# Optimization experiments

Measured on AMD Instinct MI355X. Metric: run time of the kernel, lower is better.

The kernel has to match this reference:

```python
import jax, jax.numpy as jnp
import numpy as np

H = 16
QK_NOPE = 128
QK_ROPE = 64
QK_HEAD = 192
V_HEAD = 128
KV_LORA = 512
Q_LORA = 1536
HIDDEN = 2048
ROPE_THETA = 500000.0
EPS = 1e-6


def _rms_norm(x, w, eps=EPS):
    var = jnp.mean(x * x, axis=-1, keepdims=True)
    return w * (x * jax.lax.rsqrt(var + eps))


def _rotate_half(x):
    d = x.shape[-1] // 2
    return jnp.concatenate([-x[..., d:], x[..., :d]], axis=-1)


def _rope_cos_sin(T, dim, theta, dtype):
    inv_freq = 1.0 / (theta ** (jnp.arange(0, dim, 2, dtype=jnp.float32) / dim))
    t = jnp.arange(T, dtype=jnp.float32)
    freqs = jnp.outer(t, inv_freq)               # [T, dim//2]
    emb = jnp.concatenate([freqs, freqs], axis=-1)  # [T, dim]
    return jnp.cos(emb).astype(dtype), jnp.sin(emb).astype(dtype)


def _apply_rope_interleave(q, k, cos, sin):
    # deinterleave: [x0,x1,x2,...] -> [x0,x2,... , x1,x3,...]
    def deint(x):
        return jnp.concatenate([x[..., 0::2], x[..., 1::2]], axis=-1)
    q, k = deint(q), deint(k)
    cos = cos[None, None]  # [1,1,T,d]
    sin = sin[None, None]
    q_e = q * cos + _rotate_half(q) * sin
    k_e = k * cos + _rotate_half(k) * sin
    return q_e, k_e


def setup_inputs() -> dict:
    key = jax.random.key(0)
    ks = jax.random.split(key, 8)
    s = 0.02
    B, T = 2, 2048
    return {
        "x": jax.random.normal(ks[0], (B, T, HIDDEN), jnp.float32),
        "q_a_w": jax.random.normal(ks[1], (HIDDEN, Q_LORA), jnp.float32) * s,
        "q_a_ln_w": jnp.ones((Q_LORA,), jnp.float32),
        "q_b_w": jax.random.normal(ks[2], (Q_LORA, H * QK_HEAD), jnp.float32) * s,
        "kv_a_w": jax.random.normal(ks[3], (HIDDEN, KV_LORA + QK_ROPE), jnp.float32) * s,
        "kv_a_ln_w": jnp.ones((KV_LORA,), jnp.float32),
        "kv_b_w": jax.random.normal(ks[4], (KV_LORA, H * (QK_NOPE + V_HEAD)), jnp.float32) * s,
        "o_w": jax.random.normal(ks[5], (H * V_HEAD, HIDDEN), jnp.float32) * s,
    }


def reference(x, q_a_w, q_a_ln_w, q_b_w, kv_a_w, kv_a_ln_w, kv_b_w, o_w):
    B, T, _ = x.shape
    scale = QK_HEAD ** -0.5

    # Q path: hidden -> q_lora -> RMSNorm -> H*qk_head
    q = _rms_norm(x @ q_a_w, q_a_ln_w) @ q_b_w
    q = q.reshape(B, T, H, QK_HEAD).transpose(0, 2, 1, 3)  # [B,H,T,qk_head]
    q_nope, q_rope = q[..., :QK_NOPE], q[..., QK_NOPE:]

    # KV path: hidden -> kv_lora + rope_dim
    ckv = x @ kv_a_w
    kv_c, k_rope = ckv[..., :KV_LORA], ckv[..., KV_LORA:]
    kv = _rms_norm(kv_c, kv_a_ln_w) @ kv_b_w
    kv = kv.reshape(B, T, H, QK_NOPE + V_HEAD).transpose(0, 2, 1, 3)
    k_nope, v = kv[..., :QK_NOPE], kv[..., QK_NOPE:]

    k_rope = k_rope.reshape(B, 1, T, QK_ROPE)
    cos, sin = _rope_cos_sin(T, QK_ROPE, ROPE_THETA, x.dtype)
    q_rope, k_rope = _apply_rope_interleave(q_rope, k_rope, cos, sin)
    k_rope = jnp.broadcast_to(k_rope, (B, H, T, QK_ROPE))

    qf = jnp.concatenate([q_nope, q_rope], axis=-1)  # [B,H,T,192]
    kf = jnp.concatenate([k_nope, k_rope], axis=-1)

    # causal SDPA
    scores = jnp.einsum("bhqd,bhkd->bhqk", qf, kf) * scale
    causal = jnp.tril(jnp.ones((T, T), bool))
    scores = jnp.where(causal[None, None], scores, jnp.finfo(scores.dtype).min)
    attn = jax.nn.softmax(scores, axis=-1)
    out = jnp.einsum("bhqk,bhkd->bhqd", attn, v)  # [B,H,T,128]
    out = out.transpose(0, 2, 1, 3).reshape(B, T, H * V_HEAD)
    return out @ o_w
```

## Files before the change

### kernel.cpp

```cpp
#include <hip/hip_runtime.h>
#include <hip/hip_bf16.h>
#include <cstdint>


typedef __bf16 bf16;
typedef __bf16 bf16x8 __attribute__((ext_vector_type(8)));
typedef __bf16 bf16x4v __attribute__((ext_vector_type(4)));
typedef float f32x4 __attribute__((ext_vector_type(4)));

#define TSEQ 2048
#define MR 4096

typedef const uint32_t __attribute__((address_space(1))) * gas1_t;
typedef uint32_t __attribute__((address_space(3))) * las3_t;

static __device__ __forceinline__ void gload_lds16(const void* g, void* l) {
  __builtin_amdgcn_global_load_lds(
      reinterpret_cast<gas1_t>(reinterpret_cast<uintptr_t>(g)),
      reinterpret_cast<las3_t>(reinterpret_cast<uintptr_t>(l)), 16, 0, 0);
}

static __device__ __forceinline__ f32x4 mfma16(bf16x8 a, bf16x8 b, f32x4 c) {
  return __builtin_amdgcn_mfma_f32_16x16x32_bf16(a, b, c, 0, 0, 0);
}


__global__ __launch_bounds__(256) void k_cvt_bf16(const float* __restrict__ in,
                                                  bf16* __restrict__ out) {
  int i = blockIdx.x * 256 + threadIdx.x;
  float4 f = reinterpret_cast<const float4*>(in)[i];
  bf16x4v o = {(bf16)f.x, (bf16)f.y, (bf16)f.z, (bf16)f.w};
  reinterpret_cast<bf16x4v*>(out)[i] = o;
}

__global__ __launch_bounds__(256) void k_transpose(const float* __restrict__ W,
                                                   bf16* __restrict__ Wt,
                                                   int K, int N) {
  __shared__ float t[32][33];
  int bi = blockIdx.x, bj = blockIdx.y;
  int c = threadIdx.x & 31, r0 = threadIdx.x >> 5;
#pragma unroll
  for (int rr = 0; rr < 32; rr += 8)
    t[rr + r0][c] = W[(size_t)(bj * 32 + rr + r0) * N + bi * 32 + c];
  __syncthreads();
#pragma unroll
  for (int rr = 0; rr < 32; rr += 8)
    Wt[(size_t)(bi * 32 + rr + r0) * K + bj * 32 + c] = (bf16)t[c][rr + r0];
}

__global__ __launch_bounds__(64) void k_rope_table(float* __restrict__ rt) {
  int t = blockIdx.x * 2 + (threadIdx.x >> 5);
  int j = threadIdx.x & 31;
  float freq = exp2f(-(float)j * (1.0f / 32.0f) * log2f(500000.0f));
  float ang = (float)t * freq;
  rt[t * 64 + 2 * j] = cosf(ang);
  rt[t * 64 + 2 * j + 1] = sinf(ang);
}

template <int NCH>
__global__ __launch_bounds__(64) void k_rmsnorm(const bf16* __restrict__ in,
                                                const float* __restrict__ w,
                                                bf16* __restrict__ out,
                                                int in_stride) {
  int row = blockIdx.x, lane = threadIdx.x;
  const int D = NCH * 512;
  const bf16* ip = in + (size_t)row * in_stride;
  bf16x8 v[NCH];
  float ss = 0.f;
#pragma unroll
  for (int c = 0; c < NCH; ++c) {
    v[c] = *reinterpret_cast<const bf16x8*>(ip + c * 512 + lane * 8);
#pragma unroll
    for (int e = 0; e < 8; ++e) { float f = (float)v[c][e]; ss += f * f; }
  }
#pragma unroll
  for (int m = 1; m <= 32; m <<= 1) ss += __shfl_xor(ss, m);
  float rs = rsqrtf(ss / (float)D + 1e-6f);
  bf16* op = out + (size_t)row * D;
#pragma unroll
  for (int c = 0; c < NCH; ++c) {
    bf16x8 o;
#pragma unroll
    for (int e = 0; e < 8; ++e)
      o[e] = (bf16)((float)v[c][e] * rs * w[c * 512 + lane * 8 + e]);
    *reinterpret_cast<bf16x8*>(op + c * 512 + lane * 8) = o;
  }
}

__global__ __launch_bounds__(64) void k_kv_norm_rope(
    const bf16* __restrict__ in, const float* __restrict__ w,
    const float* __restrict__ rt, bf16* __restrict__ kvn,
    bf16* __restrict__ kr, int in_stride) {
  int row = blockIdx.x, lane = threadIdx.x;
  const bf16* ip = in + (size_t)row * in_stride;
  bf16x8 v = *reinterpret_cast<const bf16x8*>(ip + lane * 8);
  float ss = 0.f;
#pragma unroll
  for (int e = 0; e < 8; ++e) { float f = (float)v[e]; ss += f * f; }
#pragma unroll
  for (int m = 1; m <= 32; m <<= 1) ss += __shfl_xor(ss, m);
  float rs = rsqrtf(ss / 512.0f + 1e-6f);
  bf16x8 o;
#pragma unroll
  for (int e = 0; e < 8; ++e) o[e] = (bf16)((float)v[e] * rs * w[lane * 8 + e]);
  *reinterpret_cast<bf16x8*>(kvn + (size_t)row * 512 + lane * 8) = o;
  if (lane < 32) {
    int t = row & (TSEQ - 1);
    float x0 = (float)ip[512 + 2 * lane], x1 = (float)ip[512 + 2 * lane + 1];
    float c = rt[t * 64 + 2 * lane], s = rt[t * 64 + 2 * lane + 1];
    kr[(size_t)row * 64 + lane] = (bf16)(x0 * c - x1 * s);
    kr[(size_t)row * 64 + 32 + lane] = (bf16)(x1 * c + x0 * s);
  }
}

__global__ __launch_bounds__(256) void k_rope_q(const bf16* __restrict__ q,
                                                const float* __restrict__ rt,
                                                bf16* __restrict__ qr) {
  int idx = blockIdx.x * 256 + threadIdx.x;
  int j = idx & 31, h = (idx >> 5) & 15, row = idx >> 9;
  int t = row & (TSEQ - 1);
  const bf16* src = q + (size_t)row * 3072 + h * 192 + 128;
  float x0 = (float)src[2 * j], x1 = (float)src[2 * j + 1];
  float c = rt[t * 64 + 2 * j], s = rt[t * 64 + 2 * j + 1];
  bf16* dst = qr + ((size_t)row * 16 + h) * 64;
  dst[j] = (bf16)(x0 * c - x1 * s);
  dst[32 + j] = (bf16)(x1 * c + x0 * s);
}

template <bool OUT_F32>
__global__ __launch_bounds__(256) void k_gemm_bt(const bf16* __restrict__ A,
                                                 const bf16* __restrict__ Bt,
                                                 void* __restrict__ C, int M,
                                                 int N, int K) {
  __shared__ bf16 As[128 * 32];
  __shared__ bf16 Bs[128 * 32];
  const int tid = threadIdx.x, lane = tid & 63, w = tid >> 6;
  const int wm = w >> 1, wn = w & 1;
  const int lg = lane >> 4, lr = lane & 15;
  const int m0 = blockIdx.y * 128, n0 = blockIdx.x * 128;
  f32x4 acc[4][4] = {};
  for (int k0 = 0; k0 < K; k0 += 32) {
    __syncthreads();
#pragma unroll
    for (int i = 0; i < 2; ++i) {
      int chunk = i * 256 + w * 64 + lane;
      int row = chunk >> 2, cc = chunk & 3;
      gload_lds16(A + (size_t)(m0 + row) * K + k0 + cc * 8,
                  (char*)As + (size_t)(i * 256 + w * 64) * 16);
      int nr = n0 + row;
      nr = nr < N ? nr : N - 1;
      gload_lds16(Bt + (size_t)nr * K + k0 + cc * 8,
                  (char*)Bs + (size_t)(i * 256 + w * 64) * 16);
    }
    __syncthreads();
    bf16x8 af[4], bfr[4];
#pragma unroll
    for (int mi = 0; mi < 4; ++mi)
      af[mi] = *reinterpret_cast<const bf16x8*>(
          &As[(wm * 64 + mi * 16 + lr) * 32 + lg * 8]);
#pragma unroll
    for (int ni = 0; ni < 4; ++ni)
      bfr[ni] = *reinterpret_cast<const bf16x8*>(
          &Bs[(wn * 64 + ni * 16 + lr) * 32 + lg * 8]);
#pragma unroll
    for (int mi = 0; mi < 4; ++mi)
#pragma unroll
      for (int ni = 0; ni < 4; ++ni)
        acc[mi][ni] = mfma16(af[mi], bfr[ni], acc[mi][ni]);
  }
#pragma unroll
  for (int mi = 0; mi < 4; ++mi)
#pragma unroll
    for (int ni = 0; ni < 4; ++ni) {
      int col = n0 + wn * 64 + ni * 16 + lr;
      if (col < N) {
#pragma unroll
        for (int r = 0; r < 4; ++r) {
          int rowg = m0 + wm * 64 + mi * 16 + lg * 4 + r;
          if (OUT_F32)
            reinterpret_cast<float*>(C)[(size_t)rowg * N + col] = acc[mi][ni][r];
          else
            reinterpret_cast<bf16*>(C)[(size_t)rowg * N + col] =
                (bf16)acc[mi][ni][r];
        }
      }
    }
}

#define GPH(BUF, MH, KH, DO_READB, STAGE_STMT, WAIT_STMT)                     \
  {                                                                           \
    if (DO_READB) {                                                           \
      _Pragma("unroll") for (int ni = 0; ni < 4; ++ni) {                      \
        int row = wn * 64 + ni * 16 + lr;                                     \
        breg[KH][ni] = *reinterpret_cast<const bf16x8*>(                      \
            &Bs[BUF][row * 64 + ((((KH)*4 + lg) ^ (row & 7)) * 8)]);          \
      }                                                                       \
    }                                                                         \
    bf16x8 af[4];                                                             \
    _Pragma("unroll") for (int mi = 0; mi < 4; ++mi) {                        \
      int row = wm * 128 + (MH)*64 + mi * 16 + lr;                            \
      af[mi] = *reinterpret_cast<const bf16x8*>(                              \
          &As[BUF][row * 64 + ((((KH)*4 + lg) ^ (row & 7)) * 8)]);            \
    }                                                                         \
    STAGE_STMT;                                                               \
    __builtin_amdgcn_s_barrier();                                             \
    __builtin_amdgcn_s_setprio(1);                                            \
    _Pragma("unroll") for (int mi = 0; mi < 4; ++mi)                          \
        _Pragma("unroll") for (int ni = 0; ni < 4; ++ni)                      \
            acc[(MH)*4 + mi][ni] =                                            \
        mfma16(af[mi], breg[KH][ni], acc[(MH)*4 + mi][ni]);                   \
    __builtin_amdgcn_s_setprio(0);                                            \
    WAIT_STMT;                                                                \
    __builtin_amdgcn_s_barrier();                                             \
  }

template <bool OUT_F32>
__global__ __launch_bounds__(512, 2) void k_gemm8(const bf16* __restrict__ A,
                                                  const bf16* __restrict__ Bt,
                                                  void* __restrict__ C, int M,
                                                  int N, int K) {
  __shared__ bf16 As[2][256 * 64];
  __shared__ bf16 Bs[2][256 * 64];
  const int tid = threadIdx.x, lane = tid & 63, w = tid >> 6;
  const int lg = lane >> 4, lr = lane & 15;
  const int wm = w >> 2, wn = w & 3;
  const int m0 = blockIdx.y * 256, n0 = blockIdx.x * 256;
  const int T = K >> 7;

  f32x4 acc[8][4] = {};
  bf16x8 breg[2][4];

  auto stageA = [&](int tau, int h) {
    char* dst = (char*)&As[tau & 1][0] + h * 16384;
#pragma unroll
    for (int j = 0; j < 2; ++j) {
      int c = j * 512 + tid;
      int row = c >> 3, slot = c & 7;
      gload_lds16(A + (size_t)(m0 + h * 128 + row) * K + tau * 64 +
                      ((slot ^ (row & 7)) * 8),
                  dst + (size_t)(j * 512 + w * 64) * 16);
    }
  };
  auto stageB = [&](int tau, int h) {
    char* dst = (char*)&Bs[tau & 1][0] + h * 16384;
#pragma unroll
    for (int j = 0; j < 2; ++j) {
      int c = j * 512 + tid;
      int row = c >> 3, slot = c & 7;
      gload_lds16(Bt + (size_t)(n0 + h * 128 + row) * K + tau * 64 +
                      ((slot ^ (row & 7)) * 8),
                  dst + (size_t)(j * 512 + w * 64) * 16);
    }
  };

  stageB(0, 0); stageB(0, 1); stageA(0, 0); stageA(0, 1);
  stageB(1, 0); stageB(1, 1); stageA(1, 0);
  asm volatile("s_waitcnt vmcnt(6)" ::: "memory");
  __builtin_amdgcn_s_barrier();

  for (int t = 0; t < T - 1; ++t) {
    const int s2 = 2 * t + 2, s3 = 2 * t + 3, a1 = 2 * t + 1;
    GPH(0, 0, 0, true,  stageA(a1, 1), ((void)0));
    GPH(0, 0, 1, true,  stageB(s2, 0), ((void)0));
    GPH(0, 1, 0, false, stageB(s2, 1), ((void)0));
    GPH(0, 1, 1, false, stageA(s2, 0),
        asm volatile("s_waitcnt vmcnt(6)" ::: "memory"));
    GPH(1, 0, 0, true,  stageA(s2, 1), ((void)0));
    GPH(1, 0, 1, true,  stageB(s3, 0), ((void)0));
    GPH(1, 1, 0, false, stageB(s3, 1), ((void)0));
    GPH(1, 1, 1, false, stageA(s3, 0),
        asm volatile("s_waitcnt vmcnt(6)" ::: "memory"));
  }
  {
    const int a1 = 2 * T - 1;
    GPH(0, 0, 0, true,  stageA(a1, 1), ((void)0));
    GPH(0, 0, 1, true,  ((void)0),     ((void)0));
    GPH(0, 1, 0, false, ((void)0),     ((void)0));
    GPH(0, 1, 1, false, ((void)0),
        asm volatile("s_waitcnt vmcnt(0)" ::: "memory"));
    GPH(1, 0, 0, true,  ((void)0), ((void)0));
    GPH(1, 0, 1, true,  ((void)0), ((void)0));
    GPH(1, 1, 0, false, ((void)0), ((void)0));
    GPH(1, 1, 1, false, ((void)0), ((void)0));
  }

#pragma unroll
  for (int mi = 0; mi < 8; ++mi)
#pragma unroll
    for (int ni = 0; ni < 4; ++ni) {
      int col = n0 + wn * 64 + ni * 16 + lr;
#pragma unroll
      for (int r = 0; r < 4; ++r) {
        int rowg = m0 + wm * 128 + mi * 16 + lg * 4 + r;
        if (OUT_F32)
          reinterpret_cast<float*>(C)[(size_t)rowg * N + col] = acc[mi][ni][r];
        else
          reinterpret_cast<bf16*>(C)[(size_t)rowg * N + col] =
              (bf16)acc[mi][ni][r];
      }
    }
}

__global__ __launch_bounds__(512, 2) void k_attn(const bf16* __restrict__ q,
                                                 const bf16* __restrict__ qr,
                                                 const bf16* __restrict__ kv,
                                                 const bf16* __restrict__ kr,
                                                 bf16* __restrict__ o) {
  __shared__ bf16 Kn[2][64 * 128];
  __shared__ bf16 Kr[2][64 * 64];
  __shared__ bf16 Vs[2][64 * 128];
  __shared__ bf16 Ps[8 * 1024];
  const int tid = threadIdx.x, lane = tid & 63, w = tid >> 6;
  const int lg = lane >> 4, lr = lane & 15;
  const float qsc = 0.07216878364870323f * 1.44269504088896f;
  uint4 vreg[2];
  const int vrr = tid & 31, vvc = tid >> 5;

  for (int t = 0; t < 2; ++t) {
    const int id = t ? 511 - (int)blockIdx.x : (int)blockIdx.x;
    const int qt = 15 - (id >> 5);
    const int bh = id & 31;
    const int b = bh >> 4, h = bh & 15;
    const int q0 = qt * 128;
    const size_t rowbase = (size_t)b * TSEQ;
    const int nkt = 2 * qt + 2;
    const int qg = q0 + w * 16 + lr;

    auto issue_loads = [&](int kbase, int buf) {
#pragma unroll
      for (int kk = 0; kk < 2; ++kk)
        vreg[kk] = *reinterpret_cast<const uint4*>(
            kv + (rowbase + kbase + vrr * 2 + kk) * 4096 + h * 256 + 128 +
            vvc * 8);
#pragma unroll
      for (int i = 0; i < 2; ++i) {
        int c = i * 512 + tid;
        int row = c >> 4, j = c & 15;
        gload_lds16(
            kv + (rowbase + kbase + row) * 4096 + h * 256 +
                ((j ^ (row & 15)) * 8),
            (char*)&Kn[buf][0] + (size_t)(i * 512 + w * 64) * 16);
      }
      {
        int row = tid >> 3, j = tid & 7;
        gload_lds16(kr + (rowbase + kbase + row) * 64 + ((j ^ (row & 7)) * 8),
                    (char*)&Kr[buf][0] + (size_t)(w * 64) * 16);
      }
    };

    auto write_vs = [&](int buf) {
      const int kb0 = vrr * 2;
      const int cC = kb0 >> 5, g = (kb0 >> 3) & 3, j0 = kb0 & 7;
      const uint32_t* r0 = reinterpret_cast<const uint32_t*>(&vreg[0]);
      const uint32_t* r1 = reinterpret_cast<const uint32_t*>(&vreg[1]);
#pragma unroll
      for (int e = 0; e < 8; ++e) {
        uint32_t h0 = (r0[e >> 1] >> ((e & 1) * 16)) & 0xffffu;
        uint32_t h1 = (r1[e >> 1] >> ((e & 1) * 16)) & 0xffffu;
        int vd = vvc * 8 + e;
        int slot = (vd & 15) ^ g;
        *reinterpret_cast<uint32_t*>(
            &Vs[buf][((cC * 8 + (vd >> 4)) * 4 + g) * 128 + slot * 8 + j0]) =
            h0 | (h1 << 16);
      }
    };

    bf16x8 qf[6];
    {
      const bf16* qp = q + (rowbase + qg) * 3072 + h * 192;
#pragma unroll
      for (int dc = 0; dc < 4; ++dc) {
        bf16x8 v = *reinterpret_cast<const bf16x8*>(qp + dc * 32 + lg * 8);
#pragma unroll
        for (int e = 0; e < 8; ++e) v[e] = (bf16)((float)v[e] * qsc);
        qf[dc] = v;
      }
      const bf16* qrp = qr + ((rowbase + qg) * 16 + h) * 64;
#pragma unroll
      for (int dc = 0; dc < 2; ++dc) {
        bf16x8 v = *reinterpret_cast<const bf16x8*>(qrp + dc * 32 + lg * 8);
#pragma unroll
        for (int e = 0; e < 8; ++e) v[e] = (bf16)((float)v[e] * qsc);
        qf[4 + dc] = v;
      }
    }

    f32x4 oacc[8] = {};
    float m_run = -1e30f, l_run = 0.f;

    issue_loads(0, 0);
    write_vs(0);
    __syncthreads();

    for (int kt = 0; kt < nkt; ++kt) {
      const int kbase = kt * 64;
      const int buf = kt & 1;
      const bool more = (kt + 1 < nkt);
      if (more) issue_loads(kbase + 64, buf ^ 1);

      if (kbase <= q0 + w * 16 + 15) {
        f32x4 sacc[4];
#pragma unroll
        for (int kb = 0; kb < 4; ++kb) {
          const int row = kb * 16 + lr;
          bf16x8 kf[6];
#pragma unroll
          for (int dc = 0; dc < 4; ++dc)
            kf[dc] = *reinterpret_cast<const bf16x8*>(
                &Kn[buf][row * 128 + (((dc * 4 + lg) ^ (row & 15)) * 8)]);
#pragma unroll
          for (int dc = 0; dc < 2; ++dc)
            kf[4 + dc] = *reinterpret_cast<const bf16x8*>(
                &Kr[buf][row * 64 + (((dc * 4 + lg) ^ (row & 7)) * 8)]);
          __builtin_amdgcn_s_setprio(1);
          f32x4 sa = {0.f, 0.f, 0.f, 0.f};
#pragma unroll
          for (int dc = 0; dc < 6; ++dc) sa = mfma16(kf[dc], qf[dc], sa);
          sacc[kb] = sa;
          __builtin_amdgcn_s_setprio(0);
        }
        float sv[4][4];
        float pmax = -1e30f;
#pragma unroll
        for (int kb = 0; kb < 4; ++kb)
#pragma unroll
          for (int r = 0; r < 4; ++r) {
            int kgl = kbase + kb * 16 + lg * 4 + r;
            float val = (kgl <= qg) ? sacc[kb][r] : -1e30f;
            sv[kb][r] = val;
            pmax = fmaxf(pmax, val);
          }
        pmax = fmaxf(pmax, __shfl_xor(pmax, 16));
        pmax = fmaxf(pmax, __shfl_xor(pmax, 32));
        float mnew = fmaxf(m_run, pmax);
        float alpha = exp2f(m_run - mnew);
        float ls = 0.f;
#pragma unroll
        for (int kb = 0; kb < 4; ++kb) {
          bf16x4v pw;
#pragma unroll
          for (int r = 0; r < 4; ++r) {
            float p = exp2f(sv[kb][r] - mnew);
            ls += p;
            pw[r] = (bf16)p;
          }
          *reinterpret_cast<bf16x4v*>(
              &Ps[w * 1024 + lr * 64 +
                  (((kb * 2 + (lg >> 1)) ^ (lr & 7)) * 8) + (lg & 1) * 4]) = pw;
        }
        ls += __shfl_xor(ls, 16);
        ls += __shfl_xor(ls, 32);
        l_run = l_run * alpha + ls;
        m_run = mnew;
#pragma unroll
        for (int vb = 0; vb < 8; ++vb) {
          oacc[vb][0] *= alpha; oacc[vb][1] *= alpha;
          oacc[vb][2] *= alpha; oacc[vb][3] *= alpha;
        }
#pragma unroll
        for (int c = 0; c < 2; ++c) {
          bf16x8 pb = *reinterpret_cast<const bf16x8*>(
              &Ps[w * 1024 + lr * 64 + (((c * 4 + lg) ^ (lr & 7)) * 8)]);
          __builtin_amdgcn_s_setprio(1);
#pragma unroll
          for (int vb = 0; vb < 8; ++vb) {
            bf16x8 av = *reinterpret_cast<const bf16x8*>(
                &Vs[buf][((c * 8 + vb) * 4 + lg) * 128 + (lr ^ lg) * 8]);
            oacc[vb] = mfma16(av, pb, oacc[vb]);
          }
          __builtin_amdgcn_s_setprio(0);
        }
      }
      if (more) write_vs(buf ^ 1);
      __syncthreads();
    }

    bf16* Os = &Kn[0][0] + w * 2048;
    {
      float inv = 1.0f / l_run;
#pragma unroll
      for (int vb = 0; vb < 8; ++vb) {
        bf16x4v ov;
#pragma unroll
        for (int r = 0; r < 4; ++r) ov[r] = (bf16)(oacc[vb][r] * inv);
        int slot16 = vb * 2 + (lg >> 1);
        *reinterpret_cast<bf16x4v*>(
            &Os[lr * 128 + ((slot16 ^ (lr & 7)) * 8) + (lg & 1) * 4]) = ov;
      }
    }
    asm volatile("s_waitcnt lgkmcnt(0)");
    __builtin_amdgcn_sched_barrier(0);
#pragma unroll
    for (int i = 0; i < 4; ++i) {
      const int r = i * 4 + lg;
      bf16x8 ov = *reinterpret_cast<const bf16x8*>(
          &Os[r * 128 + ((lr ^ (r & 7)) * 8)]);
      *reinterpret_cast<bf16x8*>(
          o + (rowbase + q0 + w * 16 + r) * 2048 + h * 128 + lr * 8) = ov;
    }
    __syncthreads();
  }
}

extern "C" void kernel_launch(void* const* d_in, const int* in_sizes, int n_in,
                              void* d_out, int out_size, void* d_ws,
                              size_t ws_size, hipStream_t stream) {
  (void)in_sizes; (void)n_in; (void)out_size; (void)ws_size;
  const float* x       = (const float*)d_in[0];
  const float* q_a_w   = (const float*)d_in[1];
  const float* q_a_ln  = (const float*)d_in[2];
  const float* q_b_w   = (const float*)d_in[3];
  const float* kv_a_w  = (const float*)d_in[4];
  const float* kv_a_ln = (const float*)d_in[5];
  const float* kv_b_w  = (const float*)d_in[6];
  const float* o_w     = (const float*)d_in[7];

  char* ws = (char*)d_ws;
  size_t off = 0;
  auto alloc = [&](size_t bytes) {
    void* p = ws + off;
    off += (bytes + 255) & ~(size_t)255;
    return p;
  };
  bf16* x_bf   = (bf16*)alloc((size_t)MR * 2048 * 2);
  bf16* ab_wt  = (bf16*)alloc((size_t)2112 * 2048 * 2);
  bf16* qb_wt  = (bf16*)alloc((size_t)3072 * 1536 * 2);
  bf16* kvb_wt = (bf16*)alloc((size_t)4096 * 512 * 2);
  bf16* o_wt   = (bf16*)alloc((size_t)2048 * 2048 * 2);
  float* rt    = (float*)alloc((size_t)2048 * 64 * 4);
  bf16* qac    = (bf16*)alloc((size_t)MR * 2112 * 2);
  bf16* q_a_n  = (bf16*)alloc((size_t)MR * 1536 * 2);
  bf16* kv_c_n = (bf16*)alloc((size_t)MR * 512 * 2);
  bf16* kr     = (bf16*)alloc((size_t)MR * 64 * 2);
  bf16* qbuf   = (bf16*)alloc((size_t)MR * 3072 * 2);
  bf16* qr     = (bf16*)alloc((size_t)MR * 16 * 64 * 2);
  bf16* kvbuf  = (bf16*)alloc((size_t)MR * 4096 * 2);
  bf16* attn_o = (bf16*)alloc((size_t)MR * 2048 * 2);

  k_cvt_bf16<<<8192, 256, 0, stream>>>(x, x_bf);
  k_transpose<<<dim3(1536 / 32, 2048 / 32), 256, 0, stream>>>(q_a_w, ab_wt, 2048, 1536);
  k_transpose<<<dim3(576 / 32, 2048 / 32), 256, 0, stream>>>(
      kv_a_w, ab_wt + (size_t)1536 * 2048, 2048, 576);
  k_transpose<<<dim3(3072 / 32, 1536 / 32), 256, 0, stream>>>(q_b_w, qb_wt, 1536, 3072);
  k_transpose<<<dim3(4096 / 32, 512 / 32), 256, 0, stream>>>(kv_b_w, kvb_wt, 512, 4096);
  k_transpose<<<dim3(2048 / 32, 2048 / 32), 256, 0, stream>>>(o_w, o_wt, 2048, 2048);
  k_rope_table<<<1024, 64, 0, stream>>>(rt);

  k_gemm_bt<false><<<dim3(17, 32), 256, 0, stream>>>(x_bf, ab_wt, qac, MR, 2112, 2048);
  k_rmsnorm<3><<<MR, 64, 0, stream>>>(qac, q_a_ln, q_a_n, 2112);
  k_kv_norm_rope<<<MR, 64, 0, stream>>>(qac + 1536, kv_a_ln, rt, kv_c_n, kr, 2112);
  k_gemm8<false><<<dim3(12, 16), 512, 0, stream>>>(q_a_n, qb_wt, qbuf, MR, 3072, 1536);
  k_rope_q<<<8192, 256, 0, stream>>>(qbuf, rt, qr);
  k_gemm8<false><<<dim3(16, 16), 512, 0, stream>>>(kv_c_n, kvb_wt, kvbuf, MR, 4096, 512);
  k_attn<<<dim3(256), 512, 0, stream>>>(qbuf, qr, kvbuf, kr, attn_o);
  k_gemm8<true><<<dim3(8, 16), 512, 0, stream>>>(attn_o, o_wt, d_out, MR, 2048, 2048);
}
```

Measured before the change: 315.7 us.

## Use tiled gemm8 for fused A-projection and skip masking and rescale in attention

Pads the fused q_a/kv_a weight to 2304 columns with a zero-filled tail so the first projection can use the larger 256x256-tile gemm8 kernel instead of the simpler 128x128 gemm_bt. In attention, tiles lying entirely below the causal diagonal skip the per-element mask. The online-softmax rescale of the accumulators is also skipped when the new max exceeds the running max by at most 8 (log2 units), a lazy-rescale trick. This cuts ALU work in the softmax loop but allows exp values up to 2^8 before the next rescale, and it adds a zero-fill launch plus wasted padded columns in the GEMM.

Result: faster. 301.2 us (median of 2 runs) (-4.6%).

```diff
diff --git a/kernel.cpp b/kernel.cpp
--- a/kernel.cpp
+++ b/kernel.cpp
@@ -31,6 +31,11 @@
   float4 f = reinterpret_cast<const float4*>(in)[i];
   bf16x4v o = {(bf16)f.x, (bf16)f.y, (bf16)f.z, (bf16)f.w};
   reinterpret_cast<bf16x4v*>(out)[i] = o;
+}
+
+__global__ __launch_bounds__(256) void k_zerofill(bf16* __restrict__ p) {
+  uint4 z = make_uint4(0, 0, 0, 0);
+  reinterpret_cast<uint4*>(p)[blockIdx.x * 256 + threadIdx.x] = z;
 }
 
 __global__ __launch_bounds__(256) void k_transpose(const float* __restrict__ W,
@@ -125,66 +130,6 @@
   bf16* dst = qr + ((size_t)row * 16 + h) * 64;
   dst[j] = (bf16)(x0 * c - x1 * s);
   dst[32 + j] = (bf16)(x1 * c + x0 * s);
-}
-
-template <bool OUT_F32>
-__global__ __launch_bounds__(256) void k_gemm_bt(const bf16* __restrict__ A,
-                                                 const bf16* __restrict__ Bt,
-                                                 void* __restrict__ C, int M,
-                                                 int N, int K) {
-  __shared__ bf16 As[128 * 32];
-  __shared__ bf16 Bs[128 * 32];
-  const int tid = threadIdx.x, lane = tid & 63, w = tid >> 6;
-  const int wm = w >> 1, wn = w & 1;
-  const int lg = lane >> 4, lr = lane & 15;
-  const int m0 = blockIdx.y * 128, n0 = blockIdx.x * 128;
-  f32x4 acc[4][4] = {};
-  for (int k0 = 0; k0 < K; k0 += 32) {
-    __syncthreads();
-#pragma unroll
-    for (int i = 0; i < 2; ++i) {
-      int chunk = i * 256 + w * 64 + lane;
-      int row = chunk >> 2, cc = chunk & 3;
-      gload_lds16(A + (size_t)(m0 + row) * K + k0 + cc * 8,
-                  (char*)As + (size_t)(i * 256 + w * 64) * 16);
-      int nr = n0 + row;
-      nr = nr < N ? nr : N - 1;
-      gload_lds16(Bt + (size_t)nr * K + k0 + cc * 8,
-                  (char*)Bs + (size_t)(i * 256 + w * 64) * 16);
-    }
-    __syncthreads();
-    bf16x8 af[4], bfr[4];
-#pragma unroll
-    for (int mi = 0; mi < 4; ++mi)
-      af[mi] = *reinterpret_cast<const bf16x8*>(
-          &As[(wm * 64 + mi * 16 + lr) * 32 + lg * 8]);
-#pragma unroll
-    for (int ni = 0; ni < 4; ++ni)
-      bfr[ni] = *reinterpret_cast<const bf16x8*>(
-          &Bs[(wn * 64 + ni * 16 + lr) * 32 + lg * 8]);
-#pragma unroll
-    for (int mi = 0; mi < 4; ++mi)
-#pragma unroll
-      for (int ni = 0; ni < 4; ++ni)
-        acc[mi][ni] = mfma16(af[mi], bfr[ni], acc[mi][ni]);
-  }
-#pragma unroll
-  for (int mi = 0; mi < 4; ++mi)
-#pragma unroll
-    for (int ni = 0; ni < 4; ++ni) {
-      int col = n0 + wn * 64 + ni * 16 + lr;
-      if (col < N) {
-#pragma unroll
-        for (int r = 0; r < 4; ++r) {
-          int rowg = m0 + wm * 64 + mi * 16 + lg * 4 + r;
-          if (OUT_F32)
-            reinterpret_cast<float*>(C)[(size_t)rowg * N + col] = acc[mi][ni][r];
-          else
-            reinterpret_cast<bf16*>(C)[(size_t)rowg * N + col] =
-                (bf16)acc[mi][ni][r];
-        }
-      }
-    }
 }
 
 #define GPH(BUF, MH, KH, DO_READB, STAGE_STMT, WAIT_STMT)                     \
@@ -420,27 +365,45 @@
           __builtin_amdgcn_s_setprio(0);
         }
         float sv[4][4];
+        if (kbase + 63 <= q0 + w * 16) {
+#pragma unroll
+          for (int kb = 0; kb < 4; ++kb)
+#pragma unroll
+            for (int r = 0; r < 4; ++r) sv[kb][r] = sacc[kb][r];
+        } else {
+#pragma unroll
+          for (int kb = 0; kb < 4; ++kb)
+#pragma unroll
+            for (int r = 0; r < 4; ++r) {
+              int kgl = kbase + kb * 16 + lg * 4 + r;
+              sv[kb][r] = (kgl <= qg) ? sacc[kb][r] : -1e30f;
+            }
+        }
         float pmax = -1e30f;
 #pragma unroll
         for (int kb = 0; kb < 4; ++kb)
 #pragma unroll
-          for (int r = 0; r < 4; ++r) {
-            int kgl = kbase + kb * 16 + lg * 4 + r;
-            float val = (kgl <= qg) ? sacc[kb][r] : -1e30f;
-            sv[kb][r] = val;
-            pmax = fmaxf(pmax, val);
-          }
+          for (int r = 0; r < 4; ++r) pmax = fmaxf(pmax, sv[kb][r]);
         pmax = fmaxf(pmax, __shfl_xor(pmax, 16));
         pmax = fmaxf(pmax, __shfl_xor(pmax, 32));
-        float mnew = fmaxf(m_run, pmax);
-        float alpha = exp2f(m_run - mnew);
+        if (!__all(pmax - m_run <= 8.0f)) {
+          float mnew = fmaxf(m_run, pmax);
+          float alpha = exp2f(m_run - mnew);
+          l_run *= alpha;
+#pragma unroll
+          for (int vb = 0; vb < 8; ++vb) {
+            oacc[vb][0] *= alpha; oacc[vb][1] *= alpha;
+            oacc[vb][2] *= alpha; oacc[vb][3] *= alpha;
+          }
+          m_run = mnew;
+        }
         float ls = 0.f;
 #pragma unroll
         for (int kb = 0; kb < 4; ++kb) {
           bf16x4v pw;
 #pragma unroll
           for (int r = 0; r < 4; ++r) {
-            float p = exp2f(sv[kb][r] - mnew);
+            float p = exp2f(sv[kb][r] - m_run);
             ls += p;
             pw[r] = (bf16)p;
           }
@@ -450,13 +413,7 @@
         }
         ls += __shfl_xor(ls, 16);
         ls += __shfl_xor(ls, 32);
-        l_run = l_run * alpha + ls;
-        m_run = mnew;
-#pragma unroll
-        for (int vb = 0; vb < 8; ++vb) {
-          oacc[vb][0] *= alpha; oacc[vb][1] *= alpha;
-          oacc[vb][2] *= alpha; oacc[vb][3] *= alpha;
-        }
+        l_run += ls;
 #pragma unroll
         for (int c = 0; c < 2; ++c) {
           bf16x8 pb = *reinterpret_cast<const bf16x8*>(
@@ -523,12 +480,12 @@
     return p;
   };
   bf16* x_bf   = (bf16*)alloc((size_t)MR * 2048 * 2);
-  bf16* ab_wt  = (bf16*)alloc((size_t)2112 * 2048 * 2);
+  bf16* ab_wt  = (bf16*)alloc((size_t)2304 * 2048 * 2);
   bf16* qb_wt  = (bf16*)alloc((size_t)3072 * 1536 * 2);
   bf16* kvb_wt = (bf16*)alloc((size_t)4096 * 512 * 2);
   bf16* o_wt   = (bf16*)alloc((size_t)2048 * 2048 * 2);
   float* rt    = (float*)alloc((size_t)2048 * 64 * 4);
-  bf16* qac    = (bf16*)alloc((size_t)MR * 2112 * 2);
+  bf16* qac    = (bf16*)alloc((size_t)MR * 2304 * 2);
   bf16* q_a_n  = (bf16*)alloc((size_t)MR * 1536 * 2);
   bf16* kv_c_n = (bf16*)alloc((size_t)MR * 512 * 2);
   bf16* kr     = (bf16*)alloc((size_t)MR * 64 * 2);
@@ -541,14 +498,15 @@
   k_transpose<<<dim3(1536 / 32, 2048 / 32), 256, 0, stream>>>(q_a_w, ab_wt, 2048, 1536);
   k_transpose<<<dim3(576 / 32, 2048 / 32), 256, 0, stream>>>(
       kv_a_w, ab_wt + (size_t)1536 * 2048, 2048, 576);
+  k_zerofill<<<192, 256, 0, stream>>>(ab_wt + (size_t)2112 * 2048);
   k_transpose<<<dim3(3072 / 32, 1536 / 32), 256, 0, stream>>>(q_b_w, qb_wt, 1536, 3072);
   k_transpose<<<dim3(4096 / 32, 512 / 32), 256, 0, stream>>>(kv_b_w, kvb_wt, 512, 4096);
   k_transpose<<<dim3(2048 / 32, 2048 / 32), 256, 0, stream>>>(o_w, o_wt, 2048, 2048);
   k_rope_table<<<1024, 64, 0, stream>>>(rt);
 
-  k_gemm_bt<false><<<dim3(17, 32), 256, 0, stream>>>(x_bf, ab_wt, qac, MR, 2112, 2048);
-  k_rmsnorm<3><<<MR, 64, 0, stream>>>(qac, q_a_ln, q_a_n, 2112);
-  k_kv_norm_rope<<<MR, 64, 0, stream>>>(qac + 1536, kv_a_ln, rt, kv_c_n, kr, 2112);
+  k_gemm8<false><<<dim3(9, 16), 512, 0, stream>>>(x_bf, ab_wt, qac, MR, 2304, 2048);
+  k_rmsnorm<3><<<MR, 64, 0, stream>>>(qac, q_a_ln, q_a_n, 2304);
+  k_kv_norm_rope<<<MR, 64, 0, stream>>>(qac + 1536, kv_a_ln, rt, kv_c_n, kr, 2304);
   k_gemm8<false><<<dim3(12, 16), 512, 0, stream>>>(q_a_n, qb_wt, qbuf, MR, 3072, 1536);
   k_rope_q<<<8192, 256, 0, stream>>>(qbuf, rt, qr);
   k_gemm8<false><<<dim3(16, 16), 512, 0, stream>>>(kv_c_n, kvb_wt, kvbuf, MR, 4096, 512);
```
